# Optimization experiments

Measured on AMD Instinct MI355X. Metric: run time of the kernel, lower is better.

Reference implementation:

```python
import jax, jax.numpy as jnp
import numpy as np

N, DIN = 8192, 768
DH1, DO1 = 64, 64
DH2, DO2 = 32, 64


def setup_inputs() -> dict:
    key = jax.random.key(0)
    ks = jax.random.split(key, 12)
    s = lambda *sh: 0.02
    inp = {
        "X": jax.random.normal(ks[0], (N, DIN), jnp.float32),
        "A": jax.random.randint(ks[1], (N, N), 0, 2, jnp.int32),
        # GAT layer 1: W (din->dh), a (2dh), W2 (dh->dout) + bias
        "W1": jax.random.normal(ks[2], (DIN, DH1), jnp.float32) * 0.02,
        "a1": jax.random.normal(ks[3], (2 * DH1,), jnp.float32) * 0.02,
        "W21": jax.random.normal(ks[4], (DH1, DO1), jnp.float32) * 0.02,
        "b21": jnp.zeros((DO1,), jnp.float32),
        # GAT layer 2
        "Wg2": jax.random.normal(ks[5], (DO1, DH2), jnp.float32) * 0.02,
        "a2": jax.random.normal(ks[6], (2 * DH2,), jnp.float32) * 0.02,
        "W22": jax.random.normal(ks[7], (DH2, DO2), jnp.float32) * 0.02,
        "b22": jnp.zeros((DO2,), jnp.float32),
        # MLP head: 64 -> 64 -> 2
        "M1": jax.random.normal(ks[8], (DO2, 64), jnp.float32) * 0.02,
        "bm1": jnp.zeros((64,), jnp.float32),
        "M2": jax.random.normal(ks[9], (64, 2), jnp.float32) * 0.02,
        "bm2": jnp.zeros((2,), jnp.float32),
    }
    return inp


def _tiny_gat(X, A, W, a, W2, b2):
    # H = X @ W; e_ij = a . [H_i, H_j] = H_i@a_src + H_j@a_dst (same math,
    # no N x N x 2dh intermediate)
    H = X @ W                      # [N, dh]
    dh = W.shape[1]
    e = (H @ a[:dh])[:, None] + (H @ a[dh:])[None, :]   # [N, N]
    e = jnp.where(A == 0, jnp.float32(-1e9), e)
    alpha = jax.nn.softmax(e, axis=1)                   # softmax over neighbors j
    Z = alpha @ H                                       # [N, dh]
    return jax.nn.elu(Z @ W2 + b2)


def reference(X, A, W1, a1, W21, b21, Wg2, a2, W22, b22, M1, bm1, M2, bm2):
    Z = _tiny_gat(X, A, W1, a1, W21, b21)    # [N, 64]
    Z = _tiny_gat(Z, A, Wg2, a2, W22, b22)   # [N, 64]
    g = Z.mean(axis=0)                       # [64]
    h = jax.nn.relu(g @ M1 + bm1)
    return h @ M2 + bm2                      # [2]
```

## Files before the change

### kernel.cpp

```cpp
#include <hip/hip_runtime.h>


#define NN 8192

typedef __attribute__((ext_vector_type(8))) short s16x8;
typedef __attribute__((ext_vector_type(4))) float f32x4;
union V16 { uint4 u; s16x8 s; };

static constexpr size_t OFF_WBITS = 0;
static constexpr size_t OFF_GT1H  = (size_t)8 << 20;
static constexpr size_t OFF_GT1L  = (size_t)9 << 20;
static constexpr size_t OFF_U1    = (size_t)10 << 20;
static constexpr size_t OFF_DEN1  = ((size_t)10 << 20) + 32 * 1024;
static constexpr size_t OFF_U2    = ((size_t)10 << 20) + 64 * 1024;
static constexpr size_t OFF_GT2H  = ((size_t)10 << 20) + 128 * 1024;
static constexpr size_t OFF_GT2L  = ((size_t)10 << 20) + 896 * 1024;
static constexpr size_t OFF_GPART = ((size_t)11 << 20) + 768 * 1024;
static constexpr size_t OFF_NUMP  = (size_t)12 << 20;

__device__ __forceinline__ float elu_f(float x) {
    return x > 0.f ? x : expm1f(x);
}
__device__ __forceinline__ unsigned int bf16_rne(float x) {
    unsigned int u = __float_as_uint(x);
    return (u + 0x7FFFu + ((u >> 16) & 1u)) >> 16;
}
__device__ __forceinline__ unsigned int split_pack(float g) {
    unsigned int hi = bf16_rne(g);
    float fhi = __uint_as_float(hi << 16);
    unsigned int lo = bf16_rne(g - fhi);
    return (hi << 16) | lo;
}

__global__ __launch_bounds__(256) void k_xw1(const float* __restrict__ X,
                                             const float* __restrict__ W1,
                                             const float* __restrict__ a1,
                                             unsigned int* __restrict__ Gt1h,
                                             unsigned int* __restrict__ Gt1l,
                                             float* __restrict__ u1) {
    __shared__ float Xt[32][65];
    __shared__ float red[32][8];
    __shared__ float us[32];
    __shared__ unsigned int Gsh[64][33];
    const int tid = threadIdx.x;
    const int row = tid & 31, cg = tid >> 5;
    const int row0 = blockIdx.x * 32;
    float acc[8];
#pragma unroll
    for (int i = 0; i < 8; ++i) acc[i] = 0.f;
    const float4* X4 = (const float4*)X;
    for (int k0 = 0; k0 < 768; k0 += 64) {
        __syncthreads();
#pragma unroll
        for (int f = tid; f < 512; f += 256) {
            int r = f >> 4, q = f & 15;
            float4 v = X4[(size_t)(row0 + r) * 192 + (k0 >> 2) + q];
            Xt[r][q * 4 + 0] = v.x; Xt[r][q * 4 + 1] = v.y;
            Xt[r][q * 4 + 2] = v.z; Xt[r][q * 4 + 3] = v.w;
        }
        __syncthreads();
        const float4* W4 = (const float4*)(W1 + (size_t)k0 * 64);
        for (int kk = 0; kk < 64; ++kk) {
            float x = Xt[row][kk];
            float4 w0 = W4[kk * 16 + cg * 2];
            float4 w1 = W4[kk * 16 + cg * 2 + 1];
            acc[0] += x * w0.x; acc[1] += x * w0.y;
            acc[2] += x * w0.z; acc[3] += x * w0.w;
            acc[4] += x * w1.x; acc[5] += x * w1.y;
            acc[6] += x * w1.z; acc[7] += x * w1.w;
        }
    }
    float p = 0.f;
#pragma unroll
    for (int i = 0; i < 8; ++i) p += acc[i] * a1[64 + cg * 8 + i];
    red[row][cg] = p;
    __syncthreads();
    if (tid < 32) {
        float d = 0.f;
#pragma unroll
        for (int g = 0; g < 8; ++g) d += red[tid][g];
        float uv = expf(d);
        u1[row0 + tid] = uv;
        us[tid] = uv;
    }
    __syncthreads();
    float uv = us[row];
#pragma unroll
    for (int i = 0; i < 8; ++i)
        Gsh[cg * 8 + i][row] = split_pack(acc[i] * uv);
    __syncthreads();
    {
        const int mt = tid >> 6, lane = tid & 63;
        const int feat = mt * 16 + (lane & 15), quad = lane >> 4;
        uint4 hv, lv;
        unsigned int g0, g1;
#define PACK_Q(Q, FX, FY)                                        \
        g0 = Gsh[feat][quad * 8 + 2 * Q];                        \
        g1 = Gsh[feat][quad * 8 + 2 * Q + 1];                    \
        hv.FX = (g0 >> 16) | (g1 & 0xFFFF0000u);                 \
        lv.FX = (g0 & 0xFFFFu) | (g1 << 16);
        PACK_Q(0, x, x) PACK_Q(1, y, y) PACK_Q(2, z, z) PACK_Q(3, w, w)
#undef PACK_Q
        size_t base = ((size_t)(mt * 256 + blockIdx.x) * 64 + lane) * 4;
        *(uint4*)(Gt1h + base) = hv;
        *(uint4*)(Gt1l + base) = lv;
    }
}

__global__ __launch_bounds__(256) void k_pack(const int* __restrict__ A,
                                              const float* __restrict__ u1,
                                              unsigned int* __restrict__ Wb32,
                                              float* __restrict__ den1) {
    __shared__ unsigned short msh[8][512];
    const int tid = threadIdx.x, wv = tid >> 6, lane = tid & 63;
    const int row0 = blockIdx.x * 8;
    float dsum0 = 0.f, dsum1 = 0.f;
    const int r0 = row0 + wv * 2, r1 = r0 + 1;
    for (int c = 0; c < 8; ++c) {
        const int j = c * 1024 + lane * 16;
        const int4* A0 = (const int4*)(A + (size_t)r0 * NN + j);
        const int4* A1 = (const int4*)(A + (size_t)r1 * NN + j);
        const float4* U4 = (const float4*)(u1 + j);
        int4 a0 = A0[0], a1 = A0[1], a2 = A0[2], a3 = A0[3];
        int4 b0 = A1[0], b1 = A1[1], b2 = A1[2], b3 = A1[3];
        float4 u0 = U4[0], u4 = U4[1], u8 = U4[2], uc = U4[3];
        unsigned int m0 = 0, m1 = 0;
#define DO4(AV, BV, UV, SH)                                            \
        m0 |= ((AV.x != 0) << (SH)) | ((AV.y != 0) << (SH + 1)) |      \
              ((AV.z != 0) << (SH + 2)) | ((AV.w != 0) << (SH + 3));   \
        m1 |= ((BV.x != 0) << (SH)) | ((BV.y != 0) << (SH + 1)) |      \
              ((BV.z != 0) << (SH + 2)) | ((BV.w != 0) << (SH + 3));   \
        dsum0 += (AV.x != 0 ? UV.x : 0.f) + (AV.y != 0 ? UV.y : 0.f) + \
                 (AV.z != 0 ? UV.z : 0.f) + (AV.w != 0 ? UV.w : 0.f);  \
        dsum1 += (BV.x != 0 ? UV.x : 0.f) + (BV.y != 0 ? UV.y : 0.f) + \
                 (BV.z != 0 ? UV.z : 0.f) + (BV.w != 0 ? UV.w : 0.f);
        DO4(a0, b0, u0, 0) DO4(a1, b1, u4, 4) DO4(a2, b2, u8, 8) DO4(a3, b3, uc, 12)
#undef DO4
        msh[wv * 2 + 0][c * 64 + lane] = (unsigned short)m0;
        msh[wv * 2 + 1][c * 64 + lane] = (unsigned short)m1;
    }
#pragma unroll
    for (int off = 32; off; off >>= 1) {
        dsum0 += __shfl_down(dsum0, off);
        dsum1 += __shfl_down(dsum1, off);
    }
    if (lane == 0) { den1[r0] = dsum0; den1[r1] = dsum1; }
    __syncthreads();
    {
        const int r = tid >> 5, i = tid & 31;
        const uint4* src = (const uint4*)&msh[r][0];
        uint4* dst = (uint4*)(Wb32 + (size_t)(row0 + r) * 256);
        dst[i] = src[i];
        dst[i + 32] = src[i + 32];
    }
}

__device__ __forceinline__ void build_lut(uint4* lut, int tid) {
    unsigned int b = (unsigned int)tid;
    uint4 e;
    e.x = ((b & 1u)   ? 0x3F80u : 0u) | ((b & 2u)   ? 0x3F800000u : 0u);
    e.y = ((b & 4u)   ? 0x3F80u : 0u) | ((b & 8u)   ? 0x3F800000u : 0u);
    e.z = ((b & 16u)  ? 0x3F80u : 0u) | ((b & 32u)  ? 0x3F800000u : 0u);
    e.w = ((b & 64u)  ? 0x3F80u : 0u) | ((b & 128u) ? 0x3F800000u : 0u);
    lut[tid] = e;
}

__global__ __launch_bounds__(256) void k_attn1(const unsigned int* __restrict__ Wb32,
                                               const unsigned int* __restrict__ Gt1h,
                                               const unsigned int* __restrict__ Gt1l,
                                               float* __restrict__ num1p) {
    __shared__ uint4 lut[256];
    __shared__ unsigned int bw[64 * 36];
    const int tid = threadIdx.x, wv = tid >> 6, lane = tid & 63;
    const int node0 = blockIdx.x * 64;
    const int kt0 = blockIdx.y * 32;
    build_lut(lut, tid);
    {
        const int r = tid >> 2, part = tid & 3;
        const uint4* src = (const uint4*)(Wb32 + (size_t)(node0 + r) * 256 + kt0 + part * 8);
        uint4 v0 = src[0], v1 = src[1];
        *(uint4*)&bw[r * 36 + part * 8] = v0;
        *(uint4*)&bw[r * 36 + part * 8 + 4] = v1;
    }
    __syncthreads();
    const int n = lane & 15, quad = lane >> 4;
    const int brow = (wv * 16 + n) * 36;
    f32x4 acc[4];
#pragma unroll
    for (int mt = 0; mt < 4; ++mt) acc[mt] = (f32x4){0.f, 0.f, 0.f, 0.f};
#pragma unroll 2
    for (int ks = 0; ks < 32; ++ks) {
        unsigned int bits = bw[brow + ks];
        unsigned int byt = (bits >> (quad * 8)) & 0xFFu;
        V16 bf; bf.u = lut[byt];
#pragma unroll
        for (int mt = 0; mt < 4; ++mt) {
            size_t base = ((size_t)(mt * 256 + kt0 + ks) * 64 + lane) * 4;
            V16 ah, al;
            ah.u = *(const uint4*)(Gt1h + base);
            al.u = *(const uint4*)(Gt1l + base);
            acc[mt] = __builtin_amdgcn_mfma_f32_16x16x32_bf16(ah.s, bf.s, acc[mt], 0, 0, 0);
            acc[mt] = __builtin_amdgcn_mfma_f32_16x16x32_bf16(al.s, bf.s, acc[mt], 0, 0, 0);
        }
    }
    const int node = node0 + wv * 16 + n;
    const int s = blockIdx.y;
#pragma unroll
    for (int mt = 0; mt < 4; ++mt)
        *(f32x4*)&num1p[((size_t)s * NN + node) * 64 + mt * 16 + quad * 4] = acc[mt];
}

__global__ __launch_bounds__(512) void k_ep1(const float* __restrict__ num1p,
                                             const float* __restrict__ den1,
                                             const float* __restrict__ W21,
                                             const float* __restrict__ b21,
                                             const float* __restrict__ Wg2,
                                             const float* __restrict__ a2,
                                             unsigned int* __restrict__ Gt2h,
                                             unsigned int* __restrict__ Gt2l,
                                             float* __restrict__ u2) {
    __shared__ float w21sh[64 * 64];
    __shared__ float wg2sh[64 * 32];
    __shared__ float zsh[8][64];
    __shared__ float osh[8][64];
    __shared__ unsigned int g2sh[32][33];
    __shared__ unsigned int u2sh[32];
    const int tid = threadIdx.x, wv = tid >> 6, lane = tid & 63;
    const int node0 = blockIdx.x * 32;
    {
        const float4* s4 = (const float4*)W21;
        float4* d4 = (float4*)w21sh;
        d4[tid] = s4[tid];
        d4[tid + 512] = s4[tid + 512];
        ((float4*)wg2sh)[tid] = ((const float4*)Wg2)[tid];
    }
    const float bb = b21[lane];
    const int l32 = lane & 31;
    const float a2v = (lane < 32) ? a2[32 + l32] : 0.f;
    __syncthreads();
    for (int it = 0; it < 4; ++it) {
        const int node = node0 + wv * 4 + it;
        float sacc = 0.f;
#pragma unroll
        for (int sp = 0; sp < 8; ++sp)
            sacc += num1p[((size_t)sp * NN + node) * 64 + lane];
        zsh[wv][lane] = sacc / den1[node];
        __syncthreads();
        float o0 = 0.f, o1 = 0.f, o2 = 0.f, o3 = 0.f;
        for (int c = 0; c < 64; c += 4) {
            o0 += zsh[wv][c + 0] * w21sh[(c + 0) * 64 + lane];
            o1 += zsh[wv][c + 1] * w21sh[(c + 1) * 64 + lane];
            o2 += zsh[wv][c + 2] * w21sh[(c + 2) * 64 + lane];
            o3 += zsh[wv][c + 3] * w21sh[(c + 3) * 64 + lane];
        }
        float o = elu_f(bb + ((o0 + o1) + (o2 + o3)));
        osh[wv][lane] = o;
        __syncthreads();
        float h0 = 0.f, h1 = 0.f;
        for (int c = 0; c < 64; c += 2) {
            h0 += osh[wv][c + 0] * wg2sh[(c + 0) * 32 + l32];
            h1 += osh[wv][c + 1] * wg2sh[(c + 1) * 32 + l32];
        }
        float hval = h0 + h1;
        float pp = hval * a2v;
#pragma unroll
        for (int off = 32; off; off >>= 1) pp += __shfl_down(pp, off);
        float d2 = __shfl(pp, 0);
        float uu = expf(d2);
        const int nodeloc = wv * 4 + it;
        if (lane == 0) {
            u2[node] = uu;
            u2sh[nodeloc] = split_pack(uu);
        }
        if (lane < 32) g2sh[l32][nodeloc] = split_pack(uu * hval);
        __syncthreads();
    }
    if (tid < 192) {
        const int mt = tid >> 6, lane2 = tid & 63;
        const int ml = lane2 & 15, quad = lane2 >> 4;
        uint4 hv, lv;
        unsigned int g0, g1;
#define PACK_Q(Q, F)                                                   \
        {                                                              \
            int j0 = quad * 8 + 2 * Q;                                 \
            if (mt < 2) { g0 = g2sh[mt * 16 + ml][j0];                 \
                          g1 = g2sh[mt * 16 + ml][j0 + 1]; }           \
            else if (ml == 0) { g0 = u2sh[j0]; g1 = u2sh[j0 + 1]; }    \
            else { g0 = 0; g1 = 0; }                                   \
            hv.F = (g0 >> 16) | (g1 & 0xFFFF0000u);                    \
            lv.F = (g0 & 0xFFFFu) | (g1 << 16);                        \
        }
        PACK_Q(0, x) PACK_Q(1, y) PACK_Q(2, z) PACK_Q(3, w)
#undef PACK_Q
        size_t base = ((size_t)(mt * 256 + blockIdx.x) * 64 + lane2) * 4;
        *(uint4*)(Gt2h + base) = hv;
        *(uint4*)(Gt2l + base) = lv;
    }
}

__global__ __launch_bounds__(256) void k_attn2(const unsigned int* __restrict__ Wb32,
                                               const unsigned int* __restrict__ Gt2h,
                                               const unsigned int* __restrict__ Gt2l,
                                               float* __restrict__ num2p) {
    __shared__ uint4 lut[256];
    __shared__ unsigned int bw[64 * 36];
    const int tid = threadIdx.x, wv = tid >> 6, lane = tid & 63;
    const int node0 = blockIdx.x * 64;
    const int kt0 = blockIdx.y * 32;
    build_lut(lut, tid);
    {
        const int r = tid >> 2, part = tid & 3;
        const uint4* src = (const uint4*)(Wb32 + (size_t)(node0 + r) * 256 + kt0 + part * 8);
        uint4 v0 = src[0], v1 = src[1];
        *(uint4*)&bw[r * 36 + part * 8] = v0;
        *(uint4*)&bw[r * 36 + part * 8 + 4] = v1;
    }
    __syncthreads();
    const int n = lane & 15, quad = lane >> 4;
    const int brow = (wv * 16 + n) * 36;
    f32x4 acc[3];
#pragma unroll
    for (int mt = 0; mt < 3; ++mt) acc[mt] = (f32x4){0.f, 0.f, 0.f, 0.f};
#pragma unroll 2
    for (int ks = 0; ks < 32; ++ks) {
        unsigned int bits = bw[brow + ks];
        unsigned int byt = (bits >> (quad * 8)) & 0xFFu;
        V16 bf; bf.u = lut[byt];
#pragma unroll
        for (int mt = 0; mt < 3; ++mt) {
            size_t base = ((size_t)(mt * 256 + kt0 + ks) * 64 + lane) * 4;
            V16 ah, al;
            ah.u = *(const uint4*)(Gt2h + base);
            al.u = *(const uint4*)(Gt2l + base);
            acc[mt] = __builtin_amdgcn_mfma_f32_16x16x32_bf16(ah.s, bf.s, acc[mt], 0, 0, 0);
            acc[mt] = __builtin_amdgcn_mfma_f32_16x16x32_bf16(al.s, bf.s, acc[mt], 0, 0, 0);
        }
    }
    const int node = node0 + wv * 16 + n;
    const int s = blockIdx.y;
#pragma unroll
    for (int mt = 0; mt < 3; ++mt)
        *(f32x4*)&num2p[((size_t)s * NN + node) * 48 + mt * 16 + quad * 4] = acc[mt];
}

__global__ __launch_bounds__(512) void k_ep2(const float* __restrict__ num2p,
                                             const float* __restrict__ W22,
                                             const float* __restrict__ b22,
                                             float* __restrict__ gpart) {
    __shared__ float w22sh[32 * 64];
    __shared__ float zsh[8][32];
    __shared__ float gsh[8][64];
    const int tid = threadIdx.x, wv = tid >> 6, lane = tid & 63;
    ((float4*)w22sh)[tid] = ((const float4*)W22)[tid];
    const float bb = b22[lane];
    __syncthreads();
    const int row = blockIdx.x * 8 + wv;
    float val = 0.f;
    if (lane < 33) {
#pragma unroll
        for (int sp = 0; sp < 8; ++sp)
            val += num2p[((size_t)sp * NN + row) * 48 + lane];
    }
    float den = __shfl(val, 32);
    if (lane < 32) zsh[wv][lane] = val / den;
    __syncthreads();
    float o0 = 0.f, o1 = 0.f;
    for (int c = 0; c < 32; c += 2) {
        o0 += zsh[wv][c + 0] * w22sh[(c + 0) * 64 + lane];
        o1 += zsh[wv][c + 1] * w22sh[(c + 1) * 64 + lane];
    }
    gsh[wv][lane] = elu_f(bb + o0 + o1);
    __syncthreads();
    if (tid < 64) {
        float s = 0.f;
#pragma unroll
        for (int w = 0; w < 8; ++w) s += gsh[w][tid];
        gpart[(size_t)blockIdx.x * 64 + tid] = s;
    }
}

__global__ __launch_bounds__(64) void k_head(const float* __restrict__ gpart,
                                             const float* __restrict__ M1,
                                             const float* __restrict__ bm1,
                                             const float* __restrict__ M2,
                                             const float* __restrict__ bm2,
                                             float* __restrict__ outp) {
    __shared__ float gsh[64];
    __shared__ float hsh[64];
    const int tid = threadIdx.x;
    float s = 0.f;
    for (int b = 0; b < 1024; ++b) s += gpart[b * 64 + tid];
    gsh[tid] = s * (1.0f / 8192.0f);
    __syncthreads();
    float h = bm1[tid];
    for (int c = 0; c < 64; ++c) h += gsh[c] * M1[c * 64 + tid];
    hsh[tid] = h > 0.f ? h : 0.f;
    __syncthreads();
    if (tid < 2) {
        float o = bm2[tid];
        for (int j = 0; j < 64; ++j) o += hsh[j] * M2[j * 2 + tid];
        outp[tid] = o;
    }
}

extern "C" void kernel_launch(void* const* d_in, const int* in_sizes, int n_in,
                              void* d_out, int out_size, void* d_ws, size_t ws_size,
                              hipStream_t stream) {
    const float* X   = (const float*)d_in[0];
    const int*   A   = (const int*)  d_in[1];
    const float* W1  = (const float*)d_in[2];
    const float* a1  = (const float*)d_in[3];
    const float* W21 = (const float*)d_in[4];
    const float* b21 = (const float*)d_in[5];
    const float* Wg2 = (const float*)d_in[6];
    const float* a2  = (const float*)d_in[7];
    const float* W22 = (const float*)d_in[8];
    const float* b22 = (const float*)d_in[9];
    const float* M1  = (const float*)d_in[10];
    const float* bm1 = (const float*)d_in[11];
    const float* M2  = (const float*)d_in[12];
    const float* bm2 = (const float*)d_in[13];
    float* out = (float*)d_out;

    char* ws = (char*)d_ws;
    unsigned int* Wbits = (unsigned int*)(ws + OFF_WBITS);
    unsigned int* Gt1h  = (unsigned int*)(ws + OFF_GT1H);
    unsigned int* Gt1l  = (unsigned int*)(ws + OFF_GT1L);
    unsigned int* Gt2h  = (unsigned int*)(ws + OFF_GT2H);
    unsigned int* Gt2l  = (unsigned int*)(ws + OFF_GT2L);
    float* u1    = (float*)(ws + OFF_U1);
    float* den1  = (float*)(ws + OFF_DEN1);
    float* u2    = (float*)(ws + OFF_U2);
    float* gpart = (float*)(ws + OFF_GPART);
    float* nump  = (float*)(ws + OFF_NUMP);

    k_xw1  <<<256, 256, 0, stream>>>(X, W1, a1, Gt1h, Gt1l, u1);
    k_pack <<<1024, 256, 0, stream>>>(A, u1, Wbits, den1);
    k_attn1<<<dim3(128, 8), 256, 0, stream>>>(Wbits, Gt1h, Gt1l, nump);
    k_ep1  <<<256, 512, 0, stream>>>(nump, den1, W21, b21, Wg2, a2, Gt2h, Gt2l, u2);
    k_attn2<<<dim3(128, 8), 256, 0, stream>>>(Wbits, Gt2h, Gt2l, nump);
    k_ep2  <<<1024, 512, 0, stream>>>(nump, W22, b22, gpart);
    k_head <<<1, 64, 0, stream>>>(gpart, M1, bm1, M2, bm2, out);
}
```

Measured before the change: 621.7 us.

## Double split-K parallelism in attention, widen xw1 and head, use wave barriers

Doubles the split-K grid of both attention kernels from 8 to 16 slices, so each block processes 16 k-steps instead of 32, and the epilogues sum 16 partials. Doubles k_xw1 threads to 512, with each thread computing 4 output columns. Replaces block-wide syncthreads in the epilogues with wave barriers where only per-wave shared data is used. Parallelizes the single-block head reduction across 4 waves and drops the unused u2 store. More partial sums raise epilogue read traffic and per-block setup (LUT build) overhead in exchange for more blocks to fill the GPU.

New measurement: 591.1 us. 4.9% less time.

```diff
diff --git a/kernel.cpp b/kernel.cpp
--- a/kernel.cpp
+++ b/kernel.cpp
@@ -12,7 +12,6 @@
 static constexpr size_t OFF_GT1L  = (size_t)9 << 20;
 static constexpr size_t OFF_U1    = (size_t)10 << 20;
 static constexpr size_t OFF_DEN1  = ((size_t)10 << 20) + 32 * 1024;
-static constexpr size_t OFF_U2    = ((size_t)10 << 20) + 64 * 1024;
 static constexpr size_t OFF_GT2H  = ((size_t)10 << 20) + 128 * 1024;
 static constexpr size_t OFF_GT2L  = ((size_t)10 << 20) + 896 * 1024;
 static constexpr size_t OFF_GPART = ((size_t)11 << 20) + 768 * 1024;
@@ -32,28 +31,27 @@
     return (hi << 16) | lo;
 }
 
-__global__ __launch_bounds__(256) void k_xw1(const float* __restrict__ X,
+__global__ __launch_bounds__(512) void k_xw1(const float* __restrict__ X,
                                              const float* __restrict__ W1,
                                              const float* __restrict__ a1,
                                              unsigned int* __restrict__ Gt1h,
                                              unsigned int* __restrict__ Gt1l,
                                              float* __restrict__ u1) {
     __shared__ float Xt[32][65];
-    __shared__ float red[32][8];
+    __shared__ float red[32][17];
     __shared__ float us[32];
     __shared__ unsigned int Gsh[64][33];
     const int tid = threadIdx.x;
     const int row = tid & 31, cg = tid >> 5;
     const int row0 = blockIdx.x * 32;
-    float acc[8];
-#pragma unroll
-    for (int i = 0; i < 8; ++i) acc[i] = 0.f;
+    float acc[4];
+#pragma unroll
+    for (int i = 0; i < 4; ++i) acc[i] = 0.f;
     const float4* X4 = (const float4*)X;
     for (int k0 = 0; k0 < 768; k0 += 64) {
         __syncthreads();
-#pragma unroll
-        for (int f = tid; f < 512; f += 256) {
-            int r = f >> 4, q = f & 15;
+        {
+            int r = tid >> 4, q = tid & 15;
             float4 v = X4[(size_t)(row0 + r) * 192 + (k0 >> 2) + q];
             Xt[r][q * 4 + 0] = v.x; Xt[r][q * 4 + 1] = v.y;
             Xt[r][q * 4 + 2] = v.z; Xt[r][q * 4 + 3] = v.w;
@@ -62,23 +60,20 @@
         const float4* W4 = (const float4*)(W1 + (size_t)k0 * 64);
         for (int kk = 0; kk < 64; ++kk) {
             float x = Xt[row][kk];
-            float4 w0 = W4[kk * 16 + cg * 2];
-            float4 w1 = W4[kk * 16 + cg * 2 + 1];
-            acc[0] += x * w0.x; acc[1] += x * w0.y;
-            acc[2] += x * w0.z; acc[3] += x * w0.w;
-            acc[4] += x * w1.x; acc[5] += x * w1.y;
-            acc[6] += x * w1.z; acc[7] += x * w1.w;
+            float4 w = W4[kk * 16 + cg];
+            acc[0] += x * w.x; acc[1] += x * w.y;
+            acc[2] += x * w.z; acc[3] += x * w.w;
         }
     }
     float p = 0.f;
 #pragma unroll
-    for (int i = 0; i < 8; ++i) p += acc[i] * a1[64 + cg * 8 + i];
+    for (int i = 0; i < 4; ++i) p += acc[i] * a1[64 + cg * 4 + i];
     red[row][cg] = p;
     __syncthreads();
     if (tid < 32) {
         float d = 0.f;
 #pragma unroll
-        for (int g = 0; g < 8; ++g) d += red[tid][g];
+        for (int g = 0; g < 16; ++g) d += red[tid][g];
         float uv = expf(d);
         u1[row0 + tid] = uv;
         us[tid] = uv;
@@ -86,20 +81,20 @@
     __syncthreads();
     float uv = us[row];
 #pragma unroll
-    for (int i = 0; i < 8; ++i)
-        Gsh[cg * 8 + i][row] = split_pack(acc[i] * uv);
-    __syncthreads();
-    {
+    for (int i = 0; i < 4; ++i)
+        Gsh[cg * 4 + i][row] = split_pack(acc[i] * uv);
+    __syncthreads();
+    if (tid < 256) {
         const int mt = tid >> 6, lane = tid & 63;
         const int feat = mt * 16 + (lane & 15), quad = lane >> 4;
         uint4 hv, lv;
         unsigned int g0, g1;
-#define PACK_Q(Q, FX, FY)                                        \
+#define PACK_Q(Q, FX)                                            \
         g0 = Gsh[feat][quad * 8 + 2 * Q];                        \
         g1 = Gsh[feat][quad * 8 + 2 * Q + 1];                    \
         hv.FX = (g0 >> 16) | (g1 & 0xFFFF0000u);                 \
         lv.FX = (g0 & 0xFFFFu) | (g1 << 16);
-        PACK_Q(0, x, x) PACK_Q(1, y, y) PACK_Q(2, z, z) PACK_Q(3, w, w)
+        PACK_Q(0, x) PACK_Q(1, y) PACK_Q(2, z) PACK_Q(3, w)
 #undef PACK_Q
         size_t base = ((size_t)(mt * 256 + blockIdx.x) * 64 + lane) * 4;
         *(uint4*)(Gt1h + base) = hv;
@@ -156,13 +151,13 @@
 }
 
 __device__ __forceinline__ void build_lut(uint4* lut, int tid) {
-    unsigned int b = (unsigned int)tid;
+    unsigned int b = (unsigned int)(tid & 255);
     uint4 e;
     e.x = ((b & 1u)   ? 0x3F80u : 0u) | ((b & 2u)   ? 0x3F800000u : 0u);
     e.y = ((b & 4u)   ? 0x3F80u : 0u) | ((b & 8u)   ? 0x3F800000u : 0u);
     e.z = ((b & 16u)  ? 0x3F80u : 0u) | ((b & 32u)  ? 0x3F800000u : 0u);
     e.w = ((b & 64u)  ? 0x3F80u : 0u) | ((b & 128u) ? 0x3F800000u : 0u);
-    lut[tid] = e;
+    if (tid < 256) lut[tid] = e;
 }
 
 __global__ __launch_bounds__(256) void k_attn1(const unsigned int* __restrict__ Wb32,
@@ -170,26 +165,24 @@
                                                const unsigned int* __restrict__ Gt1l,
                                                float* __restrict__ num1p) {
     __shared__ uint4 lut[256];
-    __shared__ unsigned int bw[64 * 36];
+    __shared__ unsigned int bw[64 * 20];
     const int tid = threadIdx.x, wv = tid >> 6, lane = tid & 63;
     const int node0 = blockIdx.x * 64;
-    const int kt0 = blockIdx.y * 32;
+    const int kt0 = blockIdx.y * 16;
     build_lut(lut, tid);
     {
         const int r = tid >> 2, part = tid & 3;
-        const uint4* src = (const uint4*)(Wb32 + (size_t)(node0 + r) * 256 + kt0 + part * 8);
-        uint4 v0 = src[0], v1 = src[1];
-        *(uint4*)&bw[r * 36 + part * 8] = v0;
-        *(uint4*)&bw[r * 36 + part * 8 + 4] = v1;
+        const uint4* src = (const uint4*)(Wb32 + (size_t)(node0 + r) * 256 + kt0 + part * 4);
+        *(uint4*)&bw[r * 20 + part * 4] = src[0];
     }
     __syncthreads();
     const int n = lane & 15, quad = lane >> 4;
-    const int brow = (wv * 16 + n) * 36;
+    const int brow = (wv * 16 + n) * 20;
     f32x4 acc[4];
 #pragma unroll
     for (int mt = 0; mt < 4; ++mt) acc[mt] = (f32x4){0.f, 0.f, 0.f, 0.f};
 #pragma unroll 2
-    for (int ks = 0; ks < 32; ++ks) {
+    for (int ks = 0; ks < 16; ++ks) {
         unsigned int bits = bw[brow + ks];
         unsigned int byt = (bits >> (quad * 8)) & 0xFFu;
         V16 bf; bf.u = lut[byt];
@@ -217,8 +210,7 @@
                                              const float* __restrict__ Wg2,
                                              const float* __restrict__ a2,
                                              unsigned int* __restrict__ Gt2h,
-                                             unsigned int* __restrict__ Gt2l,
-                                             float* __restrict__ u2) {
+                                             unsigned int* __restrict__ Gt2l) {
     __shared__ float w21sh[64 * 64];
     __shared__ float wg2sh[64 * 32];
     __shared__ float zsh[8][64];
@@ -242,10 +234,10 @@
         const int node = node0 + wv * 4 + it;
         float sacc = 0.f;
 #pragma unroll
-        for (int sp = 0; sp < 8; ++sp)
+        for (int sp = 0; sp < 16; ++sp)
             sacc += num1p[((size_t)sp * NN + node) * 64 + lane];
         zsh[wv][lane] = sacc / den1[node];
-        __syncthreads();
+        __builtin_amdgcn_wave_barrier();
         float o0 = 0.f, o1 = 0.f, o2 = 0.f, o3 = 0.f;
         for (int c = 0; c < 64; c += 4) {
             o0 += zsh[wv][c + 0] * w21sh[(c + 0) * 64 + lane];
@@ -255,7 +247,7 @@
         }
         float o = elu_f(bb + ((o0 + o1) + (o2 + o3)));
         osh[wv][lane] = o;
-        __syncthreads();
+        __builtin_amdgcn_wave_barrier();
         float h0 = 0.f, h1 = 0.f;
         for (int c = 0; c < 64; c += 2) {
             h0 += osh[wv][c + 0] * wg2sh[(c + 0) * 32 + l32];
@@ -268,13 +260,10 @@
         float d2 = __shfl(pp, 0);
         float uu = expf(d2);
         const int nodeloc = wv * 4 + it;
-        if (lane == 0) {
-            u2[node] = uu;
-            u2sh[nodeloc] = split_pack(uu);
-        }
+        if (lane == 0) u2sh[nodeloc] = split_pack(uu);
         if (lane < 32) g2sh[l32][nodeloc] = split_pack(uu * hval);
-        __syncthreads();
-    }
+    }
+    __syncthreads();
     if (tid < 192) {
         const int mt = tid >> 6, lane2 = tid & 63;
         const int ml = lane2 & 15, quad = lane2 >> 4;
@@ -303,26 +292,24 @@
                                                const unsigned int* __restrict__ Gt2l,
                                                float* __restrict__ num2p) {
     __shared__ uint4 lut[256];
-    __shared__ unsigned int bw[64 * 36];
+    __shared__ unsigned int bw[64 * 20];
     const int tid = threadIdx.x, wv = tid >> 6, lane = tid & 63;
     const int node0 = blockIdx.x * 64;
-    const int kt0 = blockIdx.y * 32;
+    const int kt0 = blockIdx.y * 16;
     build_lut(lut, tid);
     {
         const int r = tid >> 2, part = tid & 3;
-        const uint4* src = (const uint4*)(Wb32 + (size_t)(node0 + r) * 256 + kt0 + part * 8);
-        uint4 v0 = src[0], v1 = src[1];
-        *(uint4*)&bw[r * 36 + part * 8] = v0;
-        *(uint4*)&bw[r * 36 + part * 8 + 4] = v1;
+        const uint4* src = (const uint4*)(Wb32 + (size_t)(node0 + r) * 256 + kt0 + part * 4);
+        *(uint4*)&bw[r * 20 + part * 4] = src[0];
     }
     __syncthreads();
     const int n = lane & 15, quad = lane >> 4;
-    const int brow = (wv * 16 + n) * 36;
+    const int brow = (wv * 16 + n) * 20;
     f32x4 acc[3];
 #pragma unroll
     for (int mt = 0; mt < 3; ++mt) acc[mt] = (f32x4){0.f, 0.f, 0.f, 0.f};
 #pragma unroll 2
-    for (int ks = 0; ks < 32; ++ks) {
+    for (int ks = 0; ks < 16; ++ks) {
         unsigned int bits = bw[brow + ks];
         unsigned int byt = (bits >> (quad * 8)) & 0xFFu;
         V16 bf; bf.u = lut[byt];
@@ -358,12 +345,12 @@
     float val = 0.f;
     if (lane < 33) {
 #pragma unroll
-        for (int sp = 0; sp < 8; ++sp)
+        for (int sp = 0; sp < 16; ++sp)
             val += num2p[((size_t)sp * NN + row) * 48 + lane];
     }
     float den = __shfl(val, 32);
     if (lane < 32) zsh[wv][lane] = val / den;
-    __syncthreads();
+    __builtin_amdgcn_wave_barrier();
     float o0 = 0.f, o1 = 0.f;
     for (int c = 0; c < 32; c += 2) {
         o0 += zsh[wv][c + 0] * w22sh[(c + 0) * 64 + lane];
@@ -379,22 +366,30 @@
     }
 }
 
-__global__ __launch_bounds__(64) void k_head(const float* __restrict__ gpart,
-                                             const float* __restrict__ M1,
-                                             const float* __restrict__ bm1,
-                                             const float* __restrict__ M2,
-                                             const float* __restrict__ bm2,
-                                             float* __restrict__ outp) {
+__global__ __launch_bounds__(256) void k_head(const float* __restrict__ gpart,
+                                              const float* __restrict__ M1,
+                                              const float* __restrict__ bm1,
+                                              const float* __restrict__ M2,
+                                              const float* __restrict__ bm2,
+                                              float* __restrict__ outp) {
+    __shared__ float part[4][64];
     __shared__ float gsh[64];
     __shared__ float hsh[64];
-    const int tid = threadIdx.x;
+    const int tid = threadIdx.x, col = tid & 63, p = tid >> 6;
     float s = 0.f;
-    for (int b = 0; b < 1024; ++b) s += gpart[b * 64 + tid];
-    gsh[tid] = s * (1.0f / 8192.0f);
-    __syncthreads();
-    float h = bm1[tid];
-    for (int c = 0; c < 64; ++c) h += gsh[c] * M1[c * 64 + tid];
-    hsh[tid] = h > 0.f ? h : 0.f;
+    for (int b = p * 256; b < p * 256 + 256; ++b)
+        s += gpart[(size_t)b * 64 + col];
+    part[p][col] = s;
+    __syncthreads();
+    if (tid < 64)
+        gsh[tid] = (part[0][tid] + part[1][tid] + part[2][tid] + part[3][tid])
+                   * (1.0f / 8192.0f);
+    __syncthreads();
+    if (tid < 64) {
+        float h = bm1[tid];
+        for (int c = 0; c < 64; ++c) h += gsh[c] * M1[c * 64 + tid];
+        hsh[tid] = h > 0.f ? h : 0.f;
+    }
     __syncthreads();
     if (tid < 2) {
         float o = bm2[tid];
@@ -430,15 +425,14 @@
     unsigned int* Gt2l  = (unsigned int*)(ws + OFF_GT2L);
     float* u1    = (float*)(ws + OFF_U1);
     float* den1  = (float*)(ws + OFF_DEN1);
-    float* u2    = (float*)(ws + OFF_U2);
     float* gpart = (float*)(ws + OFF_GPART);
     float* nump  = (float*)(ws + OFF_NUMP);
 
-    k_xw1  <<<256, 256, 0, stream>>>(X, W1, a1, Gt1h, Gt1l, u1);
+    k_xw1  <<<256, 512, 0, stream>>>(X, W1, a1, Gt1h, Gt1l, u1);
     k_pack <<<1024, 256, 0, stream>>>(A, u1, Wbits, den1);
-    k_attn1<<<dim3(128, 8), 256, 0, stream>>>(Wbits, Gt1h, Gt1l, nump);
-    k_ep1  <<<256, 512, 0, stream>>>(nump, den1, W21, b21, Wg2, a2, Gt2h, Gt2l, u2);
-    k_attn2<<<dim3(128, 8), 256, 0, stream>>>(Wbits, Gt2h, Gt2l, nump);
+    k_attn1<<<dim3(128, 16), 256, 0, stream>>>(Wbits, Gt1h, Gt1l, nump);
+    k_ep1  <<<256, 512, 0, stream>>>(nump, den1, W21, b21, Wg2, a2, Gt2h, Gt2l);
+    k_attn2<<<dim3(128, 16), 256, 0, stream>>>(Wbits, Gt2h, Gt2l, nump);
     k_ep2  <<<1024, 512, 0, stream>>>(nump, W22, b22, gpart);
-    k_head <<<1, 64, 0, stream>>>(gpart, M1, bm1, M2, bm2, out);
-}
+    k_head <<<1, 256, 0, stream>>>(gpart, M1, bm1, M2, bm2, out);
+}
```
